# Optimization experiments

Measured on AMD Instinct MI355X. Metric: run time of the kernel, lower is better.

## Reference

```python
import jax, jax.numpy as jnp
import numpy as np


def setup_inputs() -> dict:
    key = jax.random.key(0)
    k1, k2 = jax.random.split(key)
    B, C, H, W = 1, 256, 96, 96
    C8 = C // 8
    x = jax.random.normal(k1, (B, C, H, W), dtype=jnp.float32)
    # 1x1 conv == per-pixel linear projection; weight [C8, C], bias [C8]
    w_conv = jax.random.normal(k2, (C8, C), dtype=jnp.float32) * (1.0 / np.sqrt(C))
    b_conv = jnp.zeros((C8,), dtype=jnp.float32)
    return {"x": x, "w_conv": w_conv, "b_conv": b_conv}


def reference(x, w_conv, b_conv):
    B, C, H, W = x.shape  # B must be 1 (module constraint)
    C8 = w_conv.shape[0]
    # conv_1: 1x1 conv -> [B, C8, H, W]
    x1 = jnp.einsum('bchw,oc->bohw', x, w_conv) + b_conv[None, :, None, None]
    x1 = x1.reshape(-1, H, W)                      # [C8, H, W] (B=1)
    x2 = x1.transpose(2, 1, 0).reshape(-1, C8)     # [W*H, C8], row idx = w*H + h
    x3 = x1.transpose(0, 2, 1).reshape(-1, W * H)  # [C8, W*H], col idx = w*H + h
    x4 = jax.nn.softmax(x2 @ x3, axis=-1)          # [W*H, W*H]
    x5 = x.reshape(-1, W * H)                      # [C, W*H], col idx = h*W + w
    x6 = jax.nn.softmax(x5 @ x4, axis=-1)          # [C, W*H]
    x7 = x6.reshape(B, C, H, W)
    return jax.nn.softmax(x7 + x, axis=-1)         # softmax over W
```

## Files before the change

### kernel.cpp

```cpp
#include <hip/hip_runtime.h>
#include <math.h>

#define HW 9216

typedef __attribute__((ext_vector_type(8))) short bf16x8;
typedef __attribute__((ext_vector_type(4))) float f32x4;
typedef unsigned short ushort_t;
typedef unsigned int uint_t;

__device__ __forceinline__ ushort_t f2bf(float f) {
    union { float f; uint_t u; } v; v.f = f;
    uint_t u = v.u + 0x7FFF + ((v.u >> 16) & 1);
    return (ushort_t)(u >> 16);
}

__global__ __launch_bounds__(256) void k1_conv(
        const float* __restrict__ x, const float* __restrict__ wc,
        const float* __restrict__ bc, ushort_t* __restrict__ Gbt) {
    __shared__ float wt[256][32];
    __shared__ float red[8][32][33];
    int t = threadIdx.x;
    for (int i = t; i < 256 * 32; i += 256) {
        int o = i >> 8, c = i & 255;
        wt[c][o] = wc[i];
    }
    __syncthreads();
    int px = t & 31, cg = t >> 5;
    int n = blockIdx.x * 32 + px;
    float acc[32];
    #pragma unroll
    for (int o = 0; o < 32; ++o) acc[o] = 0.f;
    int c0 = cg * 32;
    for (int cc = 0; cc < 32; ++cc) {
        int c = c0 + cc;
        float xv = x[c * HW + n];
        #pragma unroll
        for (int o4 = 0; o4 < 8; ++o4) {
            float4 wv = *(const float4*)&wt[c][o4 * 4];
            acc[o4*4+0] = fmaf(wv.x, xv, acc[o4*4+0]);
            acc[o4*4+1] = fmaf(wv.y, xv, acc[o4*4+1]);
            acc[o4*4+2] = fmaf(wv.z, xv, acc[o4*4+2]);
            acc[o4*4+3] = fmaf(wv.w, xv, acc[o4*4+3]);
        }
    }
    #pragma unroll
    for (int o = 0; o < 32; ++o) red[cg][px][o] = acc[o];
    __syncthreads();
    int px2 = t >> 3, o2 = (t & 7) * 4;
    float s[4] = {0.f, 0.f, 0.f, 0.f};
    #pragma unroll
    for (int g = 0; g < 8; ++g) {
        s[0] += red[g][px2][o2 + 0];
        s[1] += red[g][px2][o2 + 1];
        s[2] += red[g][px2][o2 + 2];
        s[3] += red[g][px2][o2 + 3];
    }
    int n2 = blockIdx.x * 32 + px2;
    int h = n2 / 96, w = n2 % 96;
    int p = w * 96 + h;
    uint2 pk;
    pk.x = (uint_t)f2bf(s[0] + bc[o2+0]) | ((uint_t)f2bf(s[1] + bc[o2+1]) << 16);
    pk.y = (uint_t)f2bf(s[2] + bc[o2+2]) | ((uint_t)f2bf(s[3] + bc[o2+3]) << 16);
    *(uint2*)&Gbt[p * 32 + o2] = pk;
}

__global__ __launch_bounds__(256) void k1b_cvt(
        const float* __restrict__ x, ushort_t* __restrict__ xbf) {
    int i = (blockIdx.x * 256 + threadIdx.x) * 8;
    float4 a = *(const float4*)&x[i];
    float4 b = *(const float4*)&x[i + 4];
    uint4 r;
    r.x = (uint_t)f2bf(a.x) | ((uint_t)f2bf(a.y) << 16);
    r.y = (uint_t)f2bf(a.z) | ((uint_t)f2bf(a.w) << 16);
    r.z = (uint_t)f2bf(b.x) | ((uint_t)f2bf(b.y) << 16);
    r.w = (uint_t)f2bf(b.z) | ((uint_t)f2bf(b.w) << 16);
    *(uint4*)&xbf[i] = r;
}

__global__ __launch_bounds__(512) void k2_stats(
        const ushort_t* __restrict__ Gbt, float* __restrict__ m_part,
        float* __restrict__ l_part) {
    __shared__ float mred[2][64], lred[2][64];
    int t = threadIdx.x;
    int w = t >> 6, l = t & 63;
    int l15 = l & 15, lg = l >> 4;
    int jb = blockIdx.x % 144, qs = blockIdx.x / 144;
    int j0 = jb * 64;
    int rf = w & 3, qp = w >> 2;
    bf16x8 aj = *(const bf16x8*)&Gbt[(j0 + rf * 16 + l15) * 32 + lg * 8];
    float m[4], lsum[4];
    #pragma unroll
    for (int r = 0; r < 4; ++r) { m[r] = -INFINITY; lsum[r] = 0.f; }
    int qbeg = qs * 1152;
    for (int tq = 0; tq < 18; ++tq) {
        int q0 = qbeg + tq * 64;
        bf16x8 b0 = *(const bf16x8*)&Gbt[(q0 + qp * 32 + l15) * 32 + lg * 8];
        bf16x8 b1 = *(const bf16x8*)&Gbt[(q0 + qp * 32 + 16 + l15) * 32 + lg * 8];
        f32x4 s0 = {0.f,0.f,0.f,0.f}, s1 = {0.f,0.f,0.f,0.f};
        s0 = __builtin_amdgcn_mfma_f32_16x16x32_bf16(aj, b0, s0, 0, 0, 0);
        s1 = __builtin_amdgcn_mfma_f32_16x16x32_bf16(aj, b1, s1, 0, 0, 0);
        #pragma unroll
        for (int r = 0; r < 4; ++r) {
            float tm = fmaxf(s0[r], s1[r]);
            float nm = fmaxf(m[r], tm);
            lsum[r] = lsum[r] * __expf(m[r] - nm)
                    + __expf(s0[r] - nm) + __expf(s1[r] - nm);
            m[r] = nm;
        }
    }
    #pragma unroll
    for (int off = 1; off < 16; off <<= 1) {
        #pragma unroll
        for (int r = 0; r < 4; ++r) {
            float mo = __shfl_xor(m[r], off);
            float lo = __shfl_xor(lsum[r], off);
            float nm = fmaxf(m[r], mo);
            lsum[r] = lsum[r] * __expf(m[r] - nm) + lo * __expf(mo - nm);
            m[r] = nm;
        }
    }
    if (l15 == 0) {
        #pragma unroll
        for (int r = 0; r < 4; ++r) {
            mred[qp][rf * 16 + lg * 4 + r] = m[r];
            lred[qp][rf * 16 + lg * 4 + r] = lsum[r];
        }
    }
    __syncthreads();
    if (t < 64) {
        float m0 = mred[0][t], m1 = mred[1][t];
        float l0 = lred[0][t], l1 = lred[1][t];
        float nm = fmaxf(m0, m1);
        float lv = l0 * __expf(m0 - nm) + l1 * __expf(m1 - nm);
        m_part[qs * HW + j0 + t] = nm;
        l_part[qs * HW + j0 + t] = lv;
    }
}

__global__ __launch_bounds__(256) void k2b_merge(
        const float* __restrict__ m_part, const float* __restrict__ l_part,
        float* __restrict__ mg, float* __restrict__ rlg) {
    int j = blockIdx.x * 256 + threadIdx.x;
    float nm = -INFINITY;
    #pragma unroll
    for (int s = 0; s < 8; ++s) nm = fmaxf(nm, m_part[s * HW + j]);
    float lv = 0.f;
    #pragma unroll
    for (int s = 0; s < 8; ++s)
        lv += l_part[s * HW + j] * __expf(m_part[s * HW + j] - nm);
    mg[j] = nm;
    rlg[j] = 1.0f / lv;
}

__global__ __launch_bounds__(256) void kzero(float* __restrict__ Z) {
    int i = blockIdx.x * 256 + threadIdx.x;
    *(float4*)&Z[i * 4] = make_float4(0.f, 0.f, 0.f, 0.f);
}

__global__ __launch_bounds__(512) void k3_pv(
        const ushort_t* __restrict__ xbf, const ushort_t* __restrict__ Gbt,
        const float* __restrict__ mg, const float* __restrict__ rlg,
        float* __restrict__ Z) {
    __shared__ ushort_t Pbt[2][64][40];
    int t = threadIdx.x;
    int w = t >> 6, l = t & 63;
    int l15 = l & 15, lg = l >> 4;
    int qb = blockIdx.x % 144, ps = blockIdx.x / 144;
    int q0 = qb * 64;
    int pf = w & 1, qf = w >> 1;
    bf16x8 bqA = *(const bf16x8*)&Gbt[(q0 + qf * 16 + l15) * 32 + lg * 8];
    f32x4 acc[2][4];
    #pragma unroll
    for (int ci = 0; ci < 2; ++ci)
        #pragma unroll
        for (int n = 0; n < 4; ++n) acc[ci][n] = (f32x4){0.f,0.f,0.f,0.f};
    const ushort_t* xrow0 = &xbf[(w * 32 + l15) * HW + lg * 8];
    const ushort_t* xrow1 = xrow0 + 16 * HW;
    int p0beg = ps * 1152;

    for (int pt = 0; pt < 36; ++pt) {
        int p0 = p0beg + pt * 32;
        int buf = pt & 1;
        bf16x8 ap = *(const bf16x8*)&Gbt[(p0 + pf * 16 + l15) * 32 + lg * 8];
        f32x4 s = {0.f,0.f,0.f,0.f};
        s = __builtin_amdgcn_mfma_f32_16x16x32_bf16(ap, bqA, s, 0, 0, 0);
        int prow = p0 + pf * 16 + lg * 4;
        float4 m4 = *(const float4*)&mg[prow];
        float4 r4 = *(const float4*)&rlg[prow];
        uint_t w0 = (uint_t)f2bf(__expf(s[0] - m4.x) * r4.x)
                  | ((uint_t)f2bf(__expf(s[1] - m4.y) * r4.y) << 16);
        uint_t w1 = (uint_t)f2bf(__expf(s[2] - m4.z) * r4.z)
                  | ((uint_t)f2bf(__expf(s[3] - m4.w) * r4.w) << 16);
        uint2 pk; pk.x = w0; pk.y = w1;
        *(uint2*)&Pbt[buf][qf * 16 + l15][pf * 16 + lg * 4] = pk;
        __syncthreads();
        bf16x8 a0 = *(const bf16x8*)&xrow0[p0];
        bf16x8 a1 = *(const bf16x8*)&xrow1[p0];
        bf16x8 b0 = *(const bf16x8*)&Pbt[buf][l15][lg * 8];
        bf16x8 b1 = *(const bf16x8*)&Pbt[buf][16 + l15][lg * 8];
        bf16x8 b2 = *(const bf16x8*)&Pbt[buf][32 + l15][lg * 8];
        bf16x8 b3 = *(const bf16x8*)&Pbt[buf][48 + l15][lg * 8];
        acc[0][0] = __builtin_amdgcn_mfma_f32_16x16x32_bf16(a0, b0, acc[0][0], 0,0,0);
        acc[0][1] = __builtin_amdgcn_mfma_f32_16x16x32_bf16(a0, b1, acc[0][1], 0,0,0);
        acc[0][2] = __builtin_amdgcn_mfma_f32_16x16x32_bf16(a0, b2, acc[0][2], 0,0,0);
        acc[0][3] = __builtin_amdgcn_mfma_f32_16x16x32_bf16(a0, b3, acc[0][3], 0,0,0);
        acc[1][0] = __builtin_amdgcn_mfma_f32_16x16x32_bf16(a1, b0, acc[1][0], 0,0,0);
        acc[1][1] = __builtin_amdgcn_mfma_f32_16x16x32_bf16(a1, b1, acc[1][1], 0,0,0);
        acc[1][2] = __builtin_amdgcn_mfma_f32_16x16x32_bf16(a1, b2, acc[1][2], 0,0,0);
        acc[1][3] = __builtin_amdgcn_mfma_f32_16x16x32_bf16(a1, b3, acc[1][3], 0,0,0);
    }
    int cbase = w * 32 + lg * 4;
    int qcol = q0 + l15;
    #pragma unroll
    for (int ci = 0; ci < 2; ++ci)
        #pragma unroll
        for (int n = 0; n < 4; ++n)
            #pragma unroll
            for (int r = 0; r < 4; ++r)
                atomicAdd(&Z[(cbase + ci * 16 + r) * HW + qcol + n * 16],
                          acc[ci][n][r]);
}

__global__ __launch_bounds__(256) void k4_softmax(
        const float* __restrict__ x, float* __restrict__ ZO) {
    __shared__ float zrow[HW];
    __shared__ float red[4];
    int t = threadIdx.x, c = blockIdx.x;
    int lane = t & 63, wid = t >> 6;
    const float* Zr = &ZO[c * HW];
    float lm = -INFINITY;
    #pragma unroll
    for (int k = 0; k < 36; ++k) {
        float v = Zr[t + 256 * k];
        zrow[t + 256 * k] = v;
        lm = fmaxf(lm, v);
    }
    #pragma unroll
    for (int off = 32; off; off >>= 1) lm = fmaxf(lm, __shfl_xor(lm, off));
    if (lane == 0) red[wid] = lm;
    __syncthreads();
    float M = fmaxf(fmaxf(red[0], red[1]), fmaxf(red[2], red[3]));
    __syncthreads();
    float ls = 0.f;
    #pragma unroll
    for (int k = 0; k < 36; ++k) {
        int i = t + 256 * k;
        float e = __expf(zrow[i] - M);
        zrow[i] = e;
        ls += e;
    }
    #pragma unroll
    for (int off = 32; off; off >>= 1) ls += __shfl_xor(ls, off);
    if (lane == 0) red[wid] = ls;
    __syncthreads();
    float rS = 1.0f / (red[0] + red[1] + red[2] + red[3]);
    const float* xr = &x[c * HW];
    float* outr = &ZO[c * HW];
    for (int kk = 0; kk < 24; ++kk) {
        int h = wid + kk * 4;
        int base = h * 96;
        float v0 = fmaf(zrow[base + lane], rS, xr[base + lane]);
        float v1 = (lane < 32)
                 ? fmaf(zrow[base + 64 + lane], rS, xr[base + 64 + lane])
                 : -INFINITY;
        float mm = fmaxf(v0, v1);
        #pragma unroll
        for (int off = 32; off; off >>= 1) mm = fmaxf(mm, __shfl_xor(mm, off));
        float e0 = __expf(v0 - mm);
        float e1 = (lane < 32) ? __expf(v1 - mm) : 0.f;
        float ss = e0 + e1;
        #pragma unroll
        for (int off = 32; off; off >>= 1) ss += __shfl_xor(ss, off);
        float r = 1.0f / ss;
        outr[base + lane] = e0 * r;
        if (lane < 32) outr[base + 64 + lane] = e1 * r;
    }
}

extern "C" void kernel_launch(void* const* d_in, const int* in_sizes, int n_in,
                              void* d_out, int out_size, void* d_ws, size_t ws_size,
                              hipStream_t stream) {
    const float* x  = (const float*)d_in[0];
    const float* wc = (const float*)d_in[1];
    const float* bc = (const float*)d_in[2];
    float* Z = (float*)d_out;

    float* m_part = (float*)d_ws;
    float* l_part = m_part + 8 * HW;
    float* mg     = l_part + 8 * HW;
    float* rlg    = mg + HW;
    ushort_t* xbf = (ushort_t*)(rlg + HW);
    ushort_t* Gbt = xbf + 256 * HW;

    k1_conv   <<<288,  256, 0, stream>>>(x, wc, bc, Gbt);
    k1b_cvt   <<<1152, 256, 0, stream>>>(x, xbf);
    k2_stats  <<<1152, 512, 0, stream>>>(Gbt, m_part, l_part);
    k2b_merge <<<36,   256, 0, stream>>>(m_part, l_part, mg, rlg);
    kzero     <<<2304, 256, 0, stream>>>(Z);
    k3_pv     <<<1152, 512, 0, stream>>>(xbf, Gbt, mg, rlg, Z);
    k4_softmax<<<256,  256, 0, stream>>>(x, Z);
}
```

Baseline: 233.2 us.

## Tile bf16 x into contiguous 32-column blocks and prefetch Gbt in PV loop

The bf16 copy of x is now written as per-32-column tiles (256 channels × 32 contiguous values), so each PV iteration reads one contiguous 16KB block instead of strided rows 18KB apart. The next iteration's Gbt fragment is prefetched, and the x loads are issued before the score MFMA, hiding global latency behind the softmax math. __syncthreads is replaced by an explicit lgkmcnt wait plus s_barrier, so outstanding global loads are not drained at the barrier. The conversion kernel now has fewer blocks, each doing strided per-channel reads, which may coalesce less well.

After: 205.5 us. -11.9%, faster.

```diff
diff --git a/kernel.cpp b/kernel.cpp
--- a/kernel.cpp
+++ b/kernel.cpp
@@ -13,6 +13,9 @@
     uint_t u = v.u + 0x7FFF + ((v.u >> 16) & 1);
     return (ushort_t)(u >> 16);
 }
+
+#define BAR() do { asm volatile("s_waitcnt lgkmcnt(0)" ::: "memory"); \
+                   __builtin_amdgcn_s_barrier(); } while (0)
 
 __global__ __launch_bounds__(256) void k1_conv(
         const float* __restrict__ x, const float* __restrict__ wc,
@@ -64,17 +67,23 @@
     *(uint2*)&Gbt[p * 32 + o2] = pk;
 }
 
-__global__ __launch_bounds__(256) void k1b_cvt(
-        const float* __restrict__ x, ushort_t* __restrict__ xbf) {
-    int i = (blockIdx.x * 256 + threadIdx.x) * 8;
-    float4 a = *(const float4*)&x[i];
-    float4 b = *(const float4*)&x[i + 4];
-    uint4 r;
-    r.x = (uint_t)f2bf(a.x) | ((uint_t)f2bf(a.y) << 16);
-    r.y = (uint_t)f2bf(a.z) | ((uint_t)f2bf(a.w) << 16);
-    r.z = (uint_t)f2bf(b.x) | ((uint_t)f2bf(b.y) << 16);
-    r.w = (uint_t)f2bf(b.z) | ((uint_t)f2bf(b.w) << 16);
-    *(uint4*)&xbf[i] = r;
+__global__ __launch_bounds__(256) void k1b_tile(
+        const float* __restrict__ x, ushort_t* __restrict__ xtile) {
+    int jt = blockIdx.x;
+    int c = threadIdx.x;
+    const float* src = &x[c * HW + jt * 32];
+    ushort_t* dst = &xtile[(jt * 256 + c) * 32];
+    #pragma unroll
+    for (int k = 0; k < 4; ++k) {
+        float4 a = *(const float4*)&src[k * 8];
+        float4 b = *(const float4*)&src[k * 8 + 4];
+        uint4 r;
+        r.x = (uint_t)f2bf(a.x) | ((uint_t)f2bf(a.y) << 16);
+        r.y = (uint_t)f2bf(a.z) | ((uint_t)f2bf(a.w) << 16);
+        r.z = (uint_t)f2bf(b.x) | ((uint_t)f2bf(b.y) << 16);
+        r.w = (uint_t)f2bf(b.z) | ((uint_t)f2bf(b.w) << 16);
+        *(uint4*)&dst[k * 8] = r;
+    }
 }
 
 __global__ __launch_bounds__(512) void k2_stats(
@@ -158,7 +167,7 @@
 }
 
 __global__ __launch_bounds__(512) void k3_pv(
-        const ushort_t* __restrict__ xbf, const ushort_t* __restrict__ Gbt,
+        const ushort_t* __restrict__ xtile, const ushort_t* __restrict__ Gbt,
         const float* __restrict__ mg, const float* __restrict__ rlg,
         float* __restrict__ Z) {
     __shared__ ushort_t Pbt[2][64][40];
@@ -174,28 +183,32 @@
     for (int ci = 0; ci < 2; ++ci)
         #pragma unroll
         for (int n = 0; n < 4; ++n) acc[ci][n] = (f32x4){0.f,0.f,0.f,0.f};
-    const ushort_t* xrow0 = &xbf[(w * 32 + l15) * HW + lg * 8];
-    const ushort_t* xrow1 = xrow0 + 16 * HW;
+    const ushort_t* xt0 = &xtile[(w * 32 + l15) * 32 + lg * 8];
+    const ushort_t* xt1 = xt0 + 16 * 32;
+    int tile0 = ps * 36;
     int p0beg = ps * 1152;
+    bf16x8 ap_c = *(const bf16x8*)&Gbt[(p0beg + pf * 16 + l15) * 32 + lg * 8];
 
     for (int pt = 0; pt < 36; ++pt) {
         int p0 = p0beg + pt * 32;
         int buf = pt & 1;
-        bf16x8 ap = *(const bf16x8*)&Gbt[(p0 + pf * 16 + l15) * 32 + lg * 8];
-        f32x4 s = {0.f,0.f,0.f,0.f};
-        s = __builtin_amdgcn_mfma_f32_16x16x32_bf16(ap, bqA, s, 0, 0, 0);
+        size_t toff = (size_t)(tile0 + pt) * 8192;
+        bf16x8 a0 = *(const bf16x8*)&xt0[toff];
+        bf16x8 a1 = *(const bf16x8*)&xt1[toff];
         int prow = p0 + pf * 16 + lg * 4;
         float4 m4 = *(const float4*)&mg[prow];
         float4 r4 = *(const float4*)&rlg[prow];
+        f32x4 s = {0.f,0.f,0.f,0.f};
+        s = __builtin_amdgcn_mfma_f32_16x16x32_bf16(ap_c, bqA, s, 0, 0, 0);
+        int pnext = (pt == 35) ? p0 : p0 + 32;
+        ap_c = *(const bf16x8*)&Gbt[(pnext + pf * 16 + l15) * 32 + lg * 8];
         uint_t w0 = (uint_t)f2bf(__expf(s[0] - m4.x) * r4.x)
                   | ((uint_t)f2bf(__expf(s[1] - m4.y) * r4.y) << 16);
         uint_t w1 = (uint_t)f2bf(__expf(s[2] - m4.z) * r4.z)
                   | ((uint_t)f2bf(__expf(s[3] - m4.w) * r4.w) << 16);
         uint2 pk; pk.x = w0; pk.y = w1;
         *(uint2*)&Pbt[buf][qf * 16 + l15][pf * 16 + lg * 4] = pk;
-        __syncthreads();
-        bf16x8 a0 = *(const bf16x8*)&xrow0[p0];
-        bf16x8 a1 = *(const bf16x8*)&xrow1[p0];
+        BAR();
         bf16x8 b0 = *(const bf16x8*)&Pbt[buf][l15][lg * 8];
         bf16x8 b1 = *(const bf16x8*)&Pbt[buf][16 + l15][lg * 8];
         bf16x8 b2 = *(const bf16x8*)&Pbt[buf][32 + l15][lg * 8];
@@ -289,14 +302,14 @@
     float* l_part = m_part + 8 * HW;
     float* mg     = l_part + 8 * HW;
     float* rlg    = mg + HW;
-    ushort_t* xbf = (ushort_t*)(rlg + HW);
-    ushort_t* Gbt = xbf + 256 * HW;
+    ushort_t* xtile = (ushort_t*)(rlg + HW);
+    ushort_t* Gbt   = xtile + 256 * HW;
 
     k1_conv   <<<288,  256, 0, stream>>>(x, wc, bc, Gbt);
-    k1b_cvt   <<<1152, 256, 0, stream>>>(x, xbf);
+    k1b_tile  <<<288,  256, 0, stream>>>(x, xtile);
     k2_stats  <<<1152, 512, 0, stream>>>(Gbt, m_part, l_part);
     k2b_merge <<<36,   256, 0, stream>>>(m_part, l_part, mg, rlg);
     kzero     <<<2304, 256, 0, stream>>>(Z);
-    k3_pv     <<<1152, 512, 0, stream>>>(xbf, Gbt, mg, rlg, Z);
+    k3_pv     <<<1152, 512, 0, stream>>>(xtile, Gbt, mg, rlg, Z);
     k4_softmax<<<256,  256, 0, stream>>>(x, Z);
 }
```
